# Optimization experiments

Hardware: AMD Instinct MI355X
Metric: run time of the kernel (lower is better)

Reference implementation:

```python
import jax, jax.numpy as jnp
import numpy as np

B, T, D = 1, 2048, 1024
H = 16
SEM_DIM, GEO_DIM, ATTN_DIM = 512, 512, 1024
ROPE_BASE = 10000.0
NEG = -1e9


def setup_inputs() -> dict:
    key = jax.random.key(0)
    ks = jax.random.split(key, 10)
    s = 0.02
    return {
        "x": jax.random.normal(ks[0], (B, T, D), jnp.float32),
        "wq_sem": jax.random.normal(ks[1], (D, SEM_DIM), jnp.float32) * s,
        "wk_sem": jax.random.normal(ks[2], (D, SEM_DIM), jnp.float32) * s,
        "wq_geo": jax.random.normal(ks[3], (D, GEO_DIM), jnp.float32) * s,
        "wk_geo": jax.random.normal(ks[4], (D, GEO_DIM), jnp.float32) * s,
        "wv": jax.random.normal(ks[5], (D, ATTN_DIM), jnp.float32) * s,
        "wo": jax.random.normal(ks[6], (ATTN_DIM, D), jnp.float32) * s,
        "k_sem_null": jax.random.normal(ks[7], (SEM_DIM,), jnp.float32) * s,
        "k_geo_null": jax.random.normal(ks[8], (GEO_DIM,), jnp.float32) * s,
        "v_null": jax.random.normal(ks[9], (ATTN_DIM,), jnp.float32) * s,
    }


def _heads(y, hd):
    b, t, _ = y.shape
    return y.reshape(b, t, H, hd).transpose(0, 2, 1, 3)  # [B,H,T,hd]


def _rope(x, cos, sin):
    # x: [B,H,T,hd], cos/sin: [T,hd//2] (rotate-half convention)
    hd = x.shape[-1]
    x1, x2 = x[..., : hd // 2], x[..., hd // 2 :]
    c = cos[None, None]
    sn = sin[None, None]
    return jnp.concatenate([x1 * c - x2 * sn, x2 * c + x1 * sn], axis=-1)


def _forward(x, wq_sem, wk_sem, wq_geo, wk_geo, wv, wo, k_sem_null, k_geo_null, v_null):
    b, t, _ = x.shape
    sem_hd = wq_sem.shape[1] // H
    geo_hd = wq_geo.shape[1] // H
    v_hd = wv.shape[1] // H
    sem_scale = 1.0 / np.sqrt(sem_hd)
    geo_scale = 1.0 / np.sqrt(geo_hd)

    qs = _heads(x @ wq_sem, sem_hd)
    ks = _heads(x @ wk_sem, sem_hd)
    qg = _heads(x @ wq_geo, geo_hd)
    kg = _heads(x @ wk_geo, geo_hd)
    v = _heads(x @ wv, v_hd)

    # RoPE on geometric branch only
    pos = jnp.arange(t, dtype=jnp.float32)
    inv_freq = 1.0 / (ROPE_BASE ** (jnp.arange(0, geo_hd, 2, dtype=jnp.float32) / geo_hd))
    ang = pos[:, None] * inv_freq[None, :]  # [T, geo_hd//2]
    cos, sin = jnp.cos(ang), jnp.sin(ang)
    qg = _rope(qg, cos, sin)
    kg = _rope(kg, cos, sin)

    # prepend null KV slot (not rotated, always attendable)
    ksn = jnp.broadcast_to(k_sem_null.reshape(1, 1, H, sem_hd).transpose(0, 2, 1, 3), (b, H, 1, sem_hd))
    kgn = jnp.broadcast_to(k_geo_null.reshape(1, 1, H, geo_hd).transpose(0, 2, 1, 3), (b, H, 1, geo_hd))
    vn = jnp.broadcast_to(v_null.reshape(1, 1, H, v_hd).transpose(0, 2, 1, 3), (b, H, 1, v_hd))
    ks_full = jnp.concatenate([ksn, ks], axis=2)  # [B,H,T+1,sem_hd]
    kg_full = jnp.concatenate([kgn, kg], axis=2)
    v_full = jnp.concatenate([vn, v], axis=2)

    # decoupled scores in fp32: sem*sem_scale + geo*geo_scale
    scores = (
        jnp.einsum("bhqd,bhkd->bhqk", qs, ks_full).astype(jnp.float32) * sem_scale
        + jnp.einsum("bhqd,bhkd->bhqk", qg, kg_full).astype(jnp.float32) * geo_scale
    )

    # causal mask over real tokens; null slot (key index 0) always visible
    causal = jnp.tril(jnp.ones((t, t), dtype=bool))
    mask = jnp.concatenate([jnp.ones((t, 1), dtype=bool), causal], axis=1)  # [T, T+1]
    scores = jnp.where(mask[None, None], scores, NEG)

    probs = jax.nn.softmax(scores, axis=-1).astype(v.dtype)
    out = jnp.einsum("bhqk,bhkd->bhqd", probs, v_full)  # [B,H,T,v_hd]
    out = out.transpose(0, 2, 1, 3).reshape(b, t, H * v_hd)
    return out @ wo


def reference(x, wq_sem, wk_sem, wq_geo, wk_geo, wv, wo, k_sem_null, k_geo_null, v_null):
    return _forward(x, wq_sem, wk_sem, wq_geo, wk_geo, wv, wo, k_sem_null, k_geo_null, v_null)
```

## Files before the change

### kernel.cpp

```cpp
#include <hip/hip_runtime.h>
#include <hip/hip_bf16.h>

typedef __hip_bfloat16 bf16;
typedef __attribute__((ext_vector_type(8))) short bf16x8;
typedef __attribute__((ext_vector_type(4))) short bf16x4;
typedef __attribute__((ext_vector_type(4))) float f32x4;

#define TSEQ   2048
#define DMODEL 1024
#define NHEAD  16
#define KST    2112
#define SCALE  0.17677669529663687f
#define LN1E4_16 0.5756462732485115f

__device__ __forceinline__ unsigned short f2bf(float f) {
    union { bf16 h; unsigned short u; } x;
    x.h = __float2bfloat16(f);
    return x.u;
}
__device__ __forceinline__ float bf2f(unsigned short u) {
    return __uint_as_float(((unsigned int)u) << 16);
}

__device__ __forceinline__ void gload_lds16(const void* g, void* l) {
    __builtin_amdgcn_global_load_lds(
        (const __attribute__((address_space(1))) void*)g,
        (__attribute__((address_space(3))) void*)l, 16, 0, 0);
}

__global__ __launch_bounds__(256) void convert_x(const float* __restrict__ X,
                                                 unsigned short* __restrict__ Xb)
{
    int i = (blockIdx.x * 256 + threadIdx.x) * 4;
    float4 v = *(const float4*)(X + i);
    ushort4 o;
    o.x = f2bf(v.x); o.y = f2bf(v.y); o.z = f2bf(v.z); o.w = f2bf(v.w);
    *(ushort4*)(Xb + i) = o;
}

__global__ __launch_bounds__(256) void transpose_all(
    const float* __restrict__ wqs, const float* __restrict__ wks,
    const float* __restrict__ wqg, const float* __restrict__ wkg,
    const float* __restrict__ wv,  const float* __restrict__ wo,
    unsigned short* __restrict__ WcatT, unsigned short* __restrict__ WoT)
{
    __shared__ float T[64][65];
    const float* src; unsigned short* dst; int C;
    switch (blockIdx.z) {
        case 0: src = wqs; dst = WcatT;               C = 512;  break;
        case 1: src = wks; dst = WcatT + 512  * 1024; C = 512;  break;
        case 2: src = wqg; dst = WcatT + 1024 * 1024; C = 512;  break;
        case 3: src = wkg; dst = WcatT + 1536 * 1024; C = 512;  break;
        case 4: src = wv;  dst = WcatT + 2048 * 1024; C = 1024; break;
        default: src = wo; dst = WoT;                 C = 1024; break;
    }
    const int c0 = blockIdx.x * 64;
    if (c0 >= C) return;
    const int r0 = blockIdx.y * 64;
    const int tid = threadIdx.x;
    #pragma unroll
    for (int i = 0; i < 16; ++i) {
        int idx = tid + 256 * i;
        int r = idx >> 6, c = idx & 63;
        T[r][c] = src[(size_t)(r0 + r) * C + c0 + c];
    }
    __syncthreads();
    #pragma unroll
    for (int i = 0; i < 16; ++i) {
        int idx = tid + 256 * i;
        int cc = idx >> 6, rr = idx & 63;
        dst[(size_t)(c0 + cc) * 1024 + r0 + rr] = f2bf(T[rr][cc]);
    }
}

__global__ __launch_bounds__(256) void init_null(
    const float* __restrict__ ksn, const float* __restrict__ kgn,
    const float* __restrict__ vn,
    unsigned short* __restrict__ Kc, unsigned short* __restrict__ Vg)
{
    const int h = blockIdx.x;
    const int tid = threadIdx.x;
    const int d = tid & 63, g = tid >> 6;
    if (g == 0)
        Kc[((size_t)h * KST + 0) * 64 + d] =
            f2bf(d < 32 ? ksn[h * 32 + d] : kgn[h * 32 + d - 32]);
    if (g == 1)
        Vg[((size_t)h * 64 + d) * KST + 0] = f2bf(vn[h * 64 + d]);
    for (int fk = 2049 + g; fk < KST; fk += 4) {
        Kc[((size_t)h * KST + fk) * 64 + d] = 0;
        Vg[((size_t)h * 64 + d) * KST + fk] = 0;
    }
}

__global__ __launch_bounds__(256) void gemm_proj_fused(
    const unsigned short* __restrict__ A,
    const unsigned short* __restrict__ Bt,
    unsigned short* __restrict__ Qc,
    unsigned short* __restrict__ Kc,
    unsigned short* __restrict__ Vg)
{
    __shared__ __align__(16) unsigned short Abuf[64 * 32];
    __shared__ __align__(16) unsigned short Bbuf[128 * 32];
    const int n0 = blockIdx.x * 128, m0 = blockIdx.y * 64;
    const int tid = threadIdx.x, l = tid & 63, wv = tid >> 6;
    const int wr = wv >> 1, wc = wv & 1;
    const int lr = l & 15, lg = l >> 4, kf = lg * 8;

    const int arow = wv * 16 + (l >> 2);
    const int aseg = (l & 3) * 8;

    f32x4 acc[2][4];
    #pragma unroll
    for (int i = 0; i < 2; ++i)
        #pragma unroll
        for (int j = 0; j < 4; ++j) acc[i][j] = (f32x4){0.f, 0.f, 0.f, 0.f};

    for (int k0 = 0; k0 < 1024; k0 += 32) {
        gload_lds16(A + (size_t)(m0 + arow) * 1024 + k0 + aseg, &Abuf[wv * 512]);
        #pragma unroll
        for (int it = 0; it < 2; ++it) {
            int brow = it * 64 + wv * 16 + (l >> 2);
            gload_lds16(Bt + (size_t)(n0 + brow) * 1024 + k0 + aseg,
                        &Bbuf[(it * 256 + wv * 64) * 8]);
        }
        __syncthreads();
        bf16x8 af[2], bfv[4];
        #pragma unroll
        for (int mf = 0; mf < 2; ++mf)
            af[mf] = *(const bf16x8*)&Abuf[(wr * 32 + mf * 16 + lr) * 32 + kf];
        #pragma unroll
        for (int nf = 0; nf < 4; ++nf)
            bfv[nf] = *(const bf16x8*)&Bbuf[(wc * 64 + nf * 16 + lr) * 32 + kf];
        #pragma unroll
        for (int mf = 0; mf < 2; ++mf)
            #pragma unroll
            for (int nf = 0; nf < 4; ++nf)
                acc[mf][nf] = __builtin_amdgcn_mfma_f32_16x16x32_bf16(
                    af[mf], bfv[nf], acc[mf][nf], 0, 0, 0);
        __syncthreads();
    }

    const int sec = n0 >> 9;
    if (sec <= 1) {
        unsigned short* dst = (sec == 0) ? Qc : Kc;
        const int tstr  = (sec == 0) ? TSEQ : KST;
        const int fkoff = (sec == 0) ? 0 : 1;
        const float sc  = (sec == 0) ? SCALE : 1.0f;
        #pragma unroll
        for (int mf = 0; mf < 2; ++mf)
            #pragma unroll
            for (int nf = 0; nf < 4; ++nf) {
                int col = (n0 & 511) + wc * 64 + nf * 16 + lr;
                int h = col >> 5, d = col & 31;
                #pragma unroll
                for (int reg = 0; reg < 4; ++reg) {
                    int q = m0 + wr * 32 + mf * 16 + lg * 4 + reg;
                    dst[((size_t)h * tstr + q + fkoff) * 64 + d] =
                        f2bf(acc[mf][nf][reg] * sc);
                }
            }
    } else if (sec <= 3) {
        unsigned short* dst = (sec == 2) ? Qc : Kc;
        const int tstr  = (sec == 2) ? TSEQ : KST;
        const int fkoff = (sec == 2) ? 0 : 1;
        const float sc  = (sec == 2) ? SCALE : 1.0f;
        const float invf = __expf(-(float)lr * LN1E4_16);
        #pragma unroll
        for (int mf = 0; mf < 2; ++mf)
            #pragma unroll
            for (int reg = 0; reg < 4; ++reg) {
                int q = m0 + wr * 32 + mf * 16 + lg * 4 + reg;
                float s, c;
                __sincosf((float)q * invf, &s, &c);
                #pragma unroll
                for (int nfp = 0; nfp < 2; ++nfp) {
                    int nf0 = nfp * 2;
                    int colbase = (n0 & 511) + wc * 64 + nf0 * 16;
                    int h = colbase >> 5;
                    float x1 = acc[mf][nf0][reg], x2 = acc[mf][nf0 + 1][reg];
                    size_t base = ((size_t)h * tstr + q + fkoff) * 64 + 32;
                    dst[base + lr]      = f2bf((x1 * c - x2 * s) * sc);
                    dst[base + lr + 16] = f2bf((x2 * c + x1 * s) * sc);
                }
            }
    } else {
        #pragma unroll
        for (int nf = 0; nf < 4; ++nf) {
            int colr = (n0 - 2048) + wc * 64 + nf * 16 + lr;
            int h = colr >> 6, dv = colr & 63;
            size_t rowbase = ((size_t)h * 64 + dv) * KST;
            #pragma unroll
            for (int mf = 0; mf < 2; ++mf)
                #pragma unroll
                for (int reg = 0; reg < 4; ++reg) {
                    int q = m0 + wr * 32 + mf * 16 + lg * 4 + reg;
                    Vg[rowbase + q + 1] = f2bf(acc[mf][nf][reg]);
                }
        }
    }
}

__global__ __launch_bounds__(256) void gemm_out(const unsigned short* __restrict__ A,
                                                const unsigned short* __restrict__ Bt,
                                                float* __restrict__ C)
{
    __shared__ __align__(16) unsigned short Abuf[64 * 32];
    __shared__ __align__(16) unsigned short Bbuf[64 * 32];
    const int n0 = blockIdx.x * 64, m0 = blockIdx.y * 64;
    const int tid = threadIdx.x, l = tid & 63, wv = tid >> 6;
    const int wr = wv >> 1, wc = wv & 1;
    const int lr = l & 15, lg = l >> 4, kf = lg * 8;

    const int arow = wv * 16 + (l >> 2);
    const int aseg = (l & 3) * 8;

    f32x4 acc[2][2];
    #pragma unroll
    for (int i = 0; i < 2; ++i)
        #pragma unroll
        for (int j = 0; j < 2; ++j) acc[i][j] = (f32x4){0.f, 0.f, 0.f, 0.f};

    for (int k0 = 0; k0 < 1024; k0 += 32) {
        gload_lds16(A  + (size_t)(m0 + arow) * 1024 + k0 + aseg, &Abuf[wv * 512]);
        gload_lds16(Bt + (size_t)(n0 + arow) * 1024 + k0 + aseg, &Bbuf[wv * 512]);
        __syncthreads();
        bf16x8 af[2], bfv[2];
        #pragma unroll
        for (int mf = 0; mf < 2; ++mf)
            af[mf] = *(const bf16x8*)&Abuf[(wr * 32 + mf * 16 + lr) * 32 + kf];
        #pragma unroll
        for (int nf = 0; nf < 2; ++nf)
            bfv[nf] = *(const bf16x8*)&Bbuf[(wc * 32 + nf * 16 + lr) * 32 + kf];
        #pragma unroll
        for (int mf = 0; mf < 2; ++mf)
            #pragma unroll
            for (int nf = 0; nf < 2; ++nf)
                acc[mf][nf] = __builtin_amdgcn_mfma_f32_16x16x32_bf16(
                    af[mf], bfv[nf], acc[mf][nf], 0, 0, 0);
        __syncthreads();
    }
    #pragma unroll
    for (int mf = 0; mf < 2; ++mf)
        #pragma unroll
        for (int nf = 0; nf < 2; ++nf)
            #pragma unroll
            for (int reg = 0; reg < 4; ++reg) {
                int row = m0 + wr * 32 + mf * 16 + lg * 4 + reg;
                int col = n0 + wc * 32 + nf * 16 + lr;
                C[(size_t)row * DMODEL + col] = acc[mf][nf][reg];
            }
}

__global__ __launch_bounds__(256) void attn_mfma(
    const unsigned short* __restrict__ Qc,
    const unsigned short* __restrict__ Kc,
    const unsigned short* __restrict__ Vg,
    unsigned short* __restrict__ attnO,
    unsigned short* __restrict__ Opart,
    float2* __restrict__ ml)
{
    __shared__ __align__(16) unsigned short KsL[2][64 * 64];
    __shared__ __align__(16) unsigned short VsL[2][64 * 64];
    __shared__ __align__(16) unsigned short Ps[64 * 64];

    const int h = blockIdx.y;
    int qb, t0, t1, part;
    bool split;
    {
        int i = blockIdx.x;
        if (i < 32) {
            split = true; qb = 31 - (i >> 1); part = i & 1;
            int nk = qb + 2, half = nk >> 1;
            t0 = part ? half : 0;
            t1 = part ? nk : half;
        } else {
            split = false; qb = 47 - i; part = 0;
            t0 = 0; t1 = qb + 2;
        }
    }
    const int q0 = qb * 64;
    const int tid = threadIdx.x, l = tid & 63, w = tid >> 6;
    const int lr = l & 15, lg = l >> 4;

    const int qrow = q0 + w * 16 + lr;
    const int d0 = lg * 8;
    bf16x8 qa0 = *(const bf16x8*)&Qc[((size_t)h * TSEQ + qrow) * 64 + d0];
    bf16x8 qa1 = *(const bf16x8*)&Qc[((size_t)h * TSEQ + qrow) * 64 + 32 + d0];

    const int sc8 = (((l & 7) ^ ((l >> 3) & 7))) * 8;
    const int r0s = (w * 2 + 0) * 8 + (l >> 3);
    const int r1s = (w * 2 + 1) * 8 + (l >> 3);
    const unsigned short* Kh = Kc + (((size_t)h * KST) << 6);
    const unsigned short* Vh = Vg + (size_t)h * 64 * KST;

#define STAGE_KV(bufi, fk0_) do {                                              \
        gload_lds16(Kh + (((size_t)((fk0_) + r0s)) << 6) + sc8,                \
                    &KsL[bufi][(w * 2 + 0) * 512]);                            \
        gload_lds16(Kh + (((size_t)((fk0_) + r1s)) << 6) + sc8,                \
                    &KsL[bufi][(w * 2 + 1) * 512]);                            \
        gload_lds16(Vh + (size_t)r0s * KST + (fk0_) + sc8,                     \
                    &VsL[bufi][(w * 2 + 0) * 512]);                            \
        gload_lds16(Vh + (size_t)r1s * KST + (fk0_) + sc8,                     \
                    &VsL[bufi][(w * 2 + 1) * 512]);                            \
    } while (0)

    f32x4 o[4];
    #pragma unroll
    for (int i = 0; i < 4; ++i) o[i] = (f32x4){0.f, 0.f, 0.f, 0.f};
    float m = -1e30f, ll = 0.0f;
    const int q = qrow;

    int buf = 0;
    STAGE_KV(0, t0 * 64);
    asm volatile("s_waitcnt vmcnt(0)" ::: "memory");
    __builtin_amdgcn_s_barrier();

    for (int kb = t0; kb < t1; ++kb) {
        const int fk0 = kb * 64;
        if (kb + 1 < t1) STAGE_KV(buf ^ 1, fk0 + 64);

        const unsigned short* Ksb = &KsL[buf][0];
        const unsigned short* Vsb = &VsL[buf][0];

        f32x4 sa[4];
        #pragma unroll
        for (int i = 0; i < 4; ++i) sa[i] = (f32x4){0.f, 0.f, 0.f, 0.f};
        __builtin_amdgcn_s_setprio(1);
        #pragma unroll
        for (int ks = 0; ks < 2; ++ks) {
            int dd = lg * 8 + ks * 32;
            bf16x8 qa = ks ? qa1 : qa0;
            #pragma unroll
            for (int nf = 0; nf < 4; ++nf) {
                int kkc = nf * 16 + lr;
                bf16x8 kbf = *(const bf16x8*)&Ksb[kkc * 64 + (dd ^ ((kkc & 7) << 3))];
                sa[nf] = __builtin_amdgcn_mfma_f32_16x16x32_bf16(kbf, qa, sa[nf], 0, 0, 0);
            }
        }
        __builtin_amdgcn_s_setprio(0);

        float sv[4][4];
        float mt = -1e30f;
        #pragma unroll
        for (int nf = 0; nf < 4; ++nf)
            #pragma unroll
            for (int reg = 0; reg < 4; ++reg) {
                int fk = fk0 + nf * 16 + lg * 4 + reg;
                float val = (fk <= q + 1) ? sa[nf][reg] : -1e9f;
                sv[nf][reg] = val;
                mt = fmaxf(mt, val);
            }
        mt = fmaxf(mt, __shfl_xor(mt, 16, 64));
        mt = fmaxf(mt, __shfl_xor(mt, 32, 64));
        float mn = fmaxf(m, mt);
        float alpha = __expf(m - mn);
        m = mn;
        float rs = 0.0f;
        #pragma unroll
        for (int nf = 0; nf < 4; ++nf)
            #pragma unroll
            for (int reg = 0; reg < 4; ++reg) {
                float p = __expf(sv[nf][reg] - m);
                sv[nf][reg] = p;
                rs += p;
            }
        rs += __shfl_xor(rs, 16, 64);
        rs += __shfl_xor(rs, 32, 64);
        ll = ll * alpha + rs;
        #pragma unroll
        for (int nf = 0; nf < 4; ++nf)
            #pragma unroll
            for (int reg = 0; reg < 4; ++reg)
                o[nf][reg] *= alpha;

        {
            int r = w * 16 + lr;
            #pragma unroll
            for (int nf = 0; nf < 4; ++nf) {
                bf16x4 pk;
                pk[0] = f2bf(sv[nf][0]); pk[1] = f2bf(sv[nf][1]);
                pk[2] = f2bf(sv[nf][2]); pk[3] = f2bf(sv[nf][3]);
                int kk0 = nf * 16 + lg * 4;
                *(bf16x4*)&Ps[r * 64 + (kk0 ^ ((r & 7) << 3))] = pk;
            }
        }

        __builtin_amdgcn_s_setprio(1);
        #pragma unroll
        for (int ks = 0; ks < 2; ++ks) {
            int kk0 = lg * 8 + ks * 32;
            int pr  = w * 16 + lr;
            bf16x8 pa = *(const bf16x8*)&Ps[pr * 64 + (kk0 ^ ((pr & 7) << 3))];
            #pragma unroll
            for (int nf = 0; nf < 4; ++nf) {
                int dv = nf * 16 + lr;
                bf16x8 vb = *(const bf16x8*)&Vsb[dv * 64 + (kk0 ^ ((dv & 7) << 3))];
                o[nf] = __builtin_amdgcn_mfma_f32_16x16x32_bf16(vb, pa, o[nf], 0, 0, 0);
            }
        }
        __builtin_amdgcn_s_setprio(0);

        asm volatile("s_waitcnt vmcnt(0)" ::: "memory");
        __builtin_amdgcn_s_barrier();
        buf ^= 1;
    }
#undef STAGE_KV

    const float inv = 1.0f / ll;
    if (!split) {
        #pragma unroll
        for (int nf = 0; nf < 4; ++nf)
            #pragma unroll
            for (int reg = 0; reg < 4; ++reg) {
                int dv = nf * 16 + lg * 4 + reg;
                attnO[(size_t)q * DMODEL + h * 64 + dv] = f2bf(o[nf][reg] * inv);
            }
    } else {
        const int sidx = (h * 16 + (qb - 16)) * 2 + part;
        unsigned short* Od = Opart + (size_t)sidx * 4096;
        const int r = w * 16 + lr;
        #pragma unroll
        for (int nf = 0; nf < 4; ++nf)
            #pragma unroll
            for (int reg = 0; reg < 4; ++reg) {
                int dv = nf * 16 + lg * 4 + reg;
                Od[r * 64 + dv] = f2bf(o[nf][reg] * inv);
            }
        if (lg == 0)
            ml[sidx * 64 + r] = make_float2(m, ll);
    }
}

__global__ __launch_bounds__(256) void combine_split(
    const unsigned short* __restrict__ Opart,
    const float2* __restrict__ ml,
    unsigned short* __restrict__ attnO)
{
    const int h = blockIdx.x >> 4, qs = blockIdx.x & 15;
    const int qb = 16 + qs;
    const int base = (h * 16 + qs) * 2;
    const unsigned short* O0 = Opart + (size_t)base * 4096;
    const unsigned short* O1 = O0 + 4096;
    const float2* ml0 = ml + base * 64;
    const float2* ml1 = ml0 + 64;
    const int t = threadIdx.x;
    const int dv = t & 63, rg = t >> 6;
    #pragma unroll
    for (int i = 0; i < 16; ++i) {
        int r = rg + i * 4;
        float2 a = ml0[r], b = ml1[r];
        float mm = fmaxf(a.x, b.x);
        float w0 = a.y * __expf(a.x - mm);
        float w1 = b.y * __expf(b.x - mm);
        float inv = 1.0f / (w0 + w1);
        float o0 = bf2f(O0[r * 64 + dv]);
        float o1 = bf2f(O1[r * 64 + dv]);
        int qq = qb * 64 + r;
        attnO[(size_t)qq * DMODEL + h * 64 + dv] = f2bf((w0 * o0 + w1 * o1) * inv);
    }
}

extern "C" void kernel_launch(void* const* d_in, const int* in_sizes, int n_in,
                              void* d_out, int out_size, void* d_ws, size_t ws_size,
                              hipStream_t stream)
{
    const float* x      = (const float*)d_in[0];
    const float* wq_sem = (const float*)d_in[1];
    const float* wk_sem = (const float*)d_in[2];
    const float* wq_geo = (const float*)d_in[3];
    const float* wk_geo = (const float*)d_in[4];
    const float* wv     = (const float*)d_in[5];
    const float* wo     = (const float*)d_in[6];
    const float* ksn    = (const float*)d_in[7];
    const float* kgn    = (const float*)d_in[8];
    const float* vn     = (const float*)d_in[9];
    float* out = (float*)d_out;

    char* ws = (char*)d_ws;
    unsigned short* Xb    = (unsigned short*)(ws);
    unsigned short* attnO = (unsigned short*)(ws);
    unsigned short* WcatT = (unsigned short*)(ws + 4194304);
    unsigned short* WoT   = (unsigned short*)(ws + 10485760);
    unsigned short* Qc    = (unsigned short*)(ws + 12582912);
    unsigned short* Kc    = (unsigned short*)(ws + 16777216);
    unsigned short* Vg    = (unsigned short*)(ws + 21102592);
    unsigned short* Opart = (unsigned short*)(ws + 25427968);
    float2*         ml    = (float2*)(ws + 29622272);

    convert_x<<<2048, 256, 0, stream>>>(x, Xb);
    transpose_all<<<dim3(16, 16, 6), 256, 0, stream>>>(
        wq_sem, wk_sem, wq_geo, wk_geo, wv, wo, WcatT, WoT);
    init_null<<<16, 256, 0, stream>>>(ksn, kgn, vn, Kc, Vg);

    gemm_proj_fused<<<dim3(24, 32), 256, 0, stream>>>(Xb, WcatT, Qc, Kc, Vg);

    attn_mfma<<<dim3(48, NHEAD), 256, 0, stream>>>(Qc, Kc, Vg, attnO, Opart, ml);
    combine_split<<<256, 256, 0, stream>>>(Opart, ml, attnO);

    gemm_out<<<dim3(16, 32), 256, 0, stream>>>(attnO, WoT, out);
}
```

Baseline: 97.32 us.

## Restructure attention into independent per-wave 16-row tasks with 1-3 way KV splits

```diff
diff --git a/kernel.cpp b/kernel.cpp
--- a/kernel.cpp
+++ b/kernel.cpp
@@ -251,7 +251,7 @@
             }
 }
 
-__global__ __launch_bounds__(256) void attn_mfma(
+__global__ __launch_bounds__(256, 3) void attn_wave(
     const unsigned short* __restrict__ Qc,
     const unsigned short* __restrict__ Kc,
     const unsigned short* __restrict__ Vg,
@@ -259,68 +259,59 @@
     unsigned short* __restrict__ Opart,
     float2* __restrict__ ml)
 {
-    __shared__ __align__(16) unsigned short KsL[2][64 * 64];
-    __shared__ __align__(16) unsigned short VsL[2][64 * 64];
-    __shared__ __align__(16) unsigned short Ps[64 * 64];
-
-    const int h = blockIdx.y;
-    int qb, t0, t1, part;
-    bool split;
-    {
-        int i = blockIdx.x;
-        if (i < 32) {
-            split = true; qb = 31 - (i >> 1); part = i & 1;
-            int nk = qb + 2, half = nk >> 1;
-            t0 = part ? half : 0;
-            t1 = part ? nk : half;
-        } else {
-            split = false; qb = 47 - i; part = 0;
-            t0 = 0; t1 = qb + 2;
-        }
-    }
-    const int q0 = qb * 64;
+    __shared__ __align__(16) unsigned short Ps[4][16 * 64];
+
     const int tid = threadIdx.x, l = tid & 63, w = tid >> 6;
     const int lr = l & 15, lg = l >> 4;
 
-    const int qrow = q0 + w * 16 + lr;
-    const int d0 = lg * 8;
-    bf16x8 qa0 = *(const bf16x8*)&Qc[((size_t)h * TSEQ + qrow) * 64 + d0];
-    bf16x8 qa1 = *(const bf16x8*)&Qc[((size_t)h * TSEQ + qrow) * 64 + 32 + d0];
-
-    const int sc8 = (((l & 7) ^ ((l >> 3) & 7))) * 8;
-    const int r0s = (w * 2 + 0) * 8 + (l >> 3);
-    const int r1s = (w * 2 + 1) * 8 + (l >> 3);
+    const int g = blockIdx.x * 4 + w;
+    const int h = g & 15;
+    const int p = 253 - (g >> 4);
+    int qsl, part, nparts;
+    if (p < 43)       { qsl = p; part = 0; nparts = 1; }
+    else if (p < 131) { int j = p - 43; qsl = 43 + (j >> 1); part = j & 1; nparts = 2; }
+    else              { int j = p - 131; qsl = 87 + j / 3; part = j % 3; nparts = 3; }
+
+    const int nt = (qsl + 1) / 4 + 1;
+    const int base = nt / nparts, rem = nt % nparts;
+    const int t0 = part * base + (part < rem ? part : rem);
+    const int t1 = t0 + base + (part < rem ? 1 : 0);
+
+    const int q = qsl * 16 + lr;
+
+    bf16x8 qa0 = *(const bf16x8*)&Qc[((size_t)h * TSEQ + q) * 64 + lg * 8];
+    bf16x8 qa1 = *(const bf16x8*)&Qc[((size_t)h * TSEQ + q) * 64 + 32 + lg * 8];
+
     const unsigned short* Kh = Kc + (((size_t)h * KST) << 6);
     const unsigned short* Vh = Vg + (size_t)h * 64 * KST;
 
-#define STAGE_KV(bufi, fk0_) do {                                              \
-        gload_lds16(Kh + (((size_t)((fk0_) + r0s)) << 6) + sc8,                \
-                    &KsL[bufi][(w * 2 + 0) * 512]);                            \
-        gload_lds16(Kh + (((size_t)((fk0_) + r1s)) << 6) + sc8,                \
-                    &KsL[bufi][(w * 2 + 1) * 512]);                            \
-        gload_lds16(Vh + (size_t)r0s * KST + (fk0_) + sc8,                     \
-                    &VsL[bufi][(w * 2 + 0) * 512]);                            \
-        gload_lds16(Vh + (size_t)r1s * KST + (fk0_) + sc8,                     \
-                    &VsL[bufi][(w * 2 + 1) * 512]);                            \
+    bf16x8 kr[8], vr[8];
+#define LOADK(fk0_) do {                                                       \
+        _Pragma("unroll")                                                      \
+        for (int ks = 0; ks < 2; ++ks)                                         \
+            _Pragma("unroll")                                                  \
+            for (int nf = 0; nf < 4; ++nf)                                     \
+                kr[ks * 4 + nf] = *(const bf16x8*)                             \
+                    &Kh[(size_t)((fk0_) + nf * 16 + lr) * 64 + lg * 8 + ks * 32]; \
+    } while (0)
+#define LOADV(fk0_) do {                                                       \
+        _Pragma("unroll")                                                      \
+        for (int ks = 0; ks < 2; ++ks)                                         \
+            _Pragma("unroll")                                                  \
+            for (int nf = 0; nf < 4; ++nf)                                     \
+                vr[ks * 4 + nf] = *(const bf16x8*)                             \
+                    &Vh[(size_t)(nf * 16 + lr) * KST + (fk0_) + lg * 8 + ks * 32]; \
     } while (0)
 
     f32x4 o[4];
     #pragma unroll
     for (int i = 0; i < 4; ++i) o[i] = (f32x4){0.f, 0.f, 0.f, 0.f};
     float m = -1e30f, ll = 0.0f;
-    const int q = qrow;
-
-    int buf = 0;
-    STAGE_KV(0, t0 * 64);
-    asm volatile("s_waitcnt vmcnt(0)" ::: "memory");
-    __builtin_amdgcn_s_barrier();
-
+
+    LOADK(t0 * 64);
     for (int kb = t0; kb < t1; ++kb) {
         const int fk0 = kb * 64;
-        if (kb + 1 < t1) STAGE_KV(buf ^ 1, fk0 + 64);
-
-        const unsigned short* Ksb = &KsL[buf][0];
-        const unsigned short* Vsb = &VsL[buf][0];
+        LOADV(fk0);
 
         f32x4 sa[4];
         #pragma unroll
@@ -328,14 +319,11 @@
         __builtin_amdgcn_s_setprio(1);
         #pragma unroll
         for (int ks = 0; ks < 2; ++ks) {
-            int dd = lg * 8 + ks * 32;
             bf16x8 qa = ks ? qa1 : qa0;
             #pragma unroll
-            for (int nf = 0; nf < 4; ++nf) {
-                int kkc = nf * 16 + lr;
-                bf16x8 kbf = *(const bf16x8*)&Ksb[kkc * 64 + (dd ^ ((kkc & 7) << 3))];
-                sa[nf] = __builtin_amdgcn_mfma_f32_16x16x32_bf16(kbf, qa, sa[nf], 0, 0, 0);
-            }
+            for (int nf = 0; nf < 4; ++nf)
+                sa[nf] = __builtin_amdgcn_mfma_f32_16x16x32_bf16(
+                    kr[ks * 4 + nf], qa, sa[nf], 0, 0, 0);
         }
         __builtin_amdgcn_s_setprio(0);
 
@@ -360,9 +348,9 @@
         for (int nf = 0; nf < 4; ++nf)
             #pragma unroll
             for (int reg = 0; reg < 4; ++reg) {
-                float p = __expf(sv[nf][reg] - m);
-                sv[nf][reg] = p;
-                rs += p;
+                float pv = __expf(sv[nf][reg] - m);
+                sv[nf][reg] = pv;
+                rs += pv;
             }
         rs += __shfl_xor(rs, 16, 64);
         rs += __shfl_xor(rs, 32, 64);
@@ -373,91 +361,98 @@
             for (int reg = 0; reg < 4; ++reg)
                 o[nf][reg] *= alpha;
 
+        #pragma unroll
+        for (int nf = 0; nf < 4; ++nf) {
+            bf16x4 pk;
+            pk[0] = f2bf(sv[nf][0]); pk[1] = f2bf(sv[nf][1]);
+            pk[2] = f2bf(sv[nf][2]); pk[3] = f2bf(sv[nf][3]);
+            int kk0 = nf * 16 + lg * 4;
+            *(bf16x4*)&Ps[w][lr * 64 + (kk0 ^ ((lr & 7) << 3))] = pk;
+        }
+
         {
-            int r = w * 16 + lr;
-            #pragma unroll
-            for (int nf = 0; nf < 4; ++nf) {
-                bf16x4 pk;
-                pk[0] = f2bf(sv[nf][0]); pk[1] = f2bf(sv[nf][1]);
-                pk[2] = f2bf(sv[nf][2]); pk[3] = f2bf(sv[nf][3]);
-                int kk0 = nf * 16 + lg * 4;
-                *(bf16x4*)&Ps[r * 64 + (kk0 ^ ((r & 7) << 3))] = pk;
-            }
+            int tn = (kb + 1 < t1) ? kb + 1 : kb;
+            LOADK(tn * 64);
         }
 
         __builtin_amdgcn_s_setprio(1);
         #pragma unroll
         for (int ks = 0; ks < 2; ++ks) {
             int kk0 = lg * 8 + ks * 32;
-            int pr  = w * 16 + lr;
-            bf16x8 pa = *(const bf16x8*)&Ps[pr * 64 + (kk0 ^ ((pr & 7) << 3))];
-            #pragma unroll
-            for (int nf = 0; nf < 4; ++nf) {
-                int dv = nf * 16 + lr;
-                bf16x8 vb = *(const bf16x8*)&Vsb[dv * 64 + (kk0 ^ ((dv & 7) << 3))];
-                o[nf] = __builtin_amdgcn_mfma_f32_16x16x32_bf16(vb, pa, o[nf], 0, 0, 0);
-            }
+            bf16x8 pa = *(const bf16x8*)&Ps[w][lr * 64 + (kk0 ^ ((lr & 7) << 3))];
+            #pragma unroll
+            for (int nf = 0; nf < 4; ++nf)
+                o[nf] = __builtin_amdgcn_mfma_f32_16x16x32_bf16(
+                    vr[ks * 4 + nf], pa, o[nf], 0, 0, 0);
         }
         __builtin_amdgcn_s_setprio(0);
-
-        asm volatile("s_waitcnt vmcnt(0)" ::: "memory");
-        __builtin_amdgcn_s_barrier();
-        buf ^= 1;
-    }
-#undef STAGE_KV
-
-    const float inv = 1.0f / ll;
-    if (!split) {
-        #pragma unroll
-        for (int nf = 0; nf < 4; ++nf)
-            #pragma unroll
-            for (int reg = 0; reg < 4; ++reg) {
-                int dv = nf * 16 + lg * 4 + reg;
-                attnO[(size_t)q * DMODEL + h * 64 + dv] = f2bf(o[nf][reg] * inv);
-            }
+    }
+#undef LOADK
+#undef LOADV
+
+    const float invl = 1.0f / ll;
+    if (nparts == 1) {
+        #pragma unroll
+        for (int nf = 0; nf < 4; ++nf) {
+            ushort4 ov;
+            ov.x = f2bf(o[nf][0] * invl); ov.y = f2bf(o[nf][1] * invl);
+            ov.z = f2bf(o[nf][2] * invl); ov.w = f2bf(o[nf][3] * invl);
+            *(ushort4*)&attnO[(size_t)q * DMODEL + h * 64 + nf * 16 + lg * 4] = ov;
+        }
     } else {
-        const int sidx = (h * 16 + (qb - 16)) * 2 + part;
-        unsigned short* Od = Opart + (size_t)sidx * 4096;
-        const int r = w * 16 + lr;
-        #pragma unroll
-        for (int nf = 0; nf < 4; ++nf)
-            #pragma unroll
-            for (int reg = 0; reg < 4; ++reg) {
-                int dv = nf * 16 + lg * 4 + reg;
-                Od[r * 64 + dv] = f2bf(o[nf][reg] * inv);
-            }
+        int local = (nparts == 2) ? (qsl - 43) * 2 + part
+                                  : 88 + (qsl - 87) * 3 + part;
+        int sidx = h * 211 + local;
+        unsigned short* Od = Opart + (size_t)sidx * 1024;
+        #pragma unroll
+        for (int nf = 0; nf < 4; ++nf) {
+            ushort4 ov;
+            ov.x = f2bf(o[nf][0] * invl); ov.y = f2bf(o[nf][1] * invl);
+            ov.z = f2bf(o[nf][2] * invl); ov.w = f2bf(o[nf][3] * invl);
+            *(ushort4*)&Od[lr * 64 + nf * 16 + lg * 4] = ov;
+        }
         if (lg == 0)
-            ml[sidx * 64 + r] = make_float2(m, ll);
-    }
-}
-
-__global__ __launch_bounds__(256) void combine_split(
+            ml[sidx * 16 + lr] = make_float2(m, ll);
+    }
+}
+
+__global__ __launch_bounds__(256) void combine_wave(
     const unsigned short* __restrict__ Opart,
     const float2* __restrict__ ml,
     unsigned short* __restrict__ attnO)
 {
-    const int h = blockIdx.x >> 4, qs = blockIdx.x & 15;
-    const int qb = 16 + qs;
-    const int base = (h * 16 + qs) * 2;
-    const unsigned short* O0 = Opart + (size_t)base * 4096;
-    const unsigned short* O1 = O0 + 4096;
-    const float2* ml0 = ml + base * 64;
-    const float2* ml1 = ml0 + 64;
+    const int bx = blockIdx.x;
+    const int h = bx / 85, qsl = 43 + bx % 85;
+    const int nparts = (qsl < 87) ? 2 : 3;
+    const int local0 = (qsl < 87) ? (qsl - 43) * 2 : 88 + (qsl - 87) * 3;
+    const int sidx0 = h * 211 + local0;
     const int t = threadIdx.x;
-    const int dv = t & 63, rg = t >> 6;
-    #pragma unroll
-    for (int i = 0; i < 16; ++i) {
-        int r = rg + i * 4;
-        float2 a = ml0[r], b = ml1[r];
-        float mm = fmaxf(a.x, b.x);
-        float w0 = a.y * __expf(a.x - mm);
-        float w1 = b.y * __expf(b.x - mm);
-        float inv = 1.0f / (w0 + w1);
-        float o0 = bf2f(O0[r * 64 + dv]);
-        float o1 = bf2f(O1[r * 64 + dv]);
-        int qq = qb * 64 + r;
-        attnO[(size_t)qq * DMODEL + h * 64 + dv] = f2bf((w0 * o0 + w1 * o1) * inv);
-    }
+    const int r = t >> 4, dv0 = (t & 15) * 4;
+
+    float2 m0 = ml[(sidx0 + 0) * 16 + r];
+    float2 m1 = ml[(sidx0 + 1) * 16 + r];
+    float2 m2 = (nparts == 3) ? ml[(sidx0 + 2) * 16 + r] : make_float2(-1e30f, 0.f);
+    float mm = fmaxf(fmaxf(m0.x, m1.x), m2.x);
+    float w0 = m0.y * __expf(m0.x - mm);
+    float w1 = m1.y * __expf(m1.x - mm);
+    float w2 = m2.y * __expf(m2.x - mm);
+    float inv = 1.0f / (w0 + w1 + w2);
+
+    const unsigned short* O0 = Opart + (size_t)(sidx0 + 0) * 1024 + r * 64 + dv0;
+    const unsigned short* O1 = Opart + (size_t)(sidx0 + 1) * 1024 + r * 64 + dv0;
+    const unsigned short* O2 = (nparts == 3)
+        ? Opart + (size_t)(sidx0 + 2) * 1024 + r * 64 + dv0 : O0;
+
+    ushort4 a = *(const ushort4*)O0;
+    ushort4 b = *(const ushort4*)O1;
+    ushort4 c = *(const ushort4*)O2;
+    ushort4 ov;
+    ov.x = f2bf((w0 * bf2f(a.x) + w1 * bf2f(b.x) + w2 * bf2f(c.x)) * inv);
+    ov.y = f2bf((w0 * bf2f(a.y) + w1 * bf2f(b.y) + w2 * bf2f(c.y)) * inv);
+    ov.z = f2bf((w0 * bf2f(a.z) + w1 * bf2f(b.z) + w2 * bf2f(c.z)) * inv);
+    ov.w = f2bf((w0 * bf2f(a.w) + w1 * bf2f(b.w) + w2 * bf2f(c.w)) * inv);
+    int q = qsl * 16 + r;
+    *(ushort4*)&attnO[(size_t)q * DMODEL + h * 64 + dv0] = ov;
 }
 
 extern "C" void kernel_launch(void* const* d_in, const int* in_sizes, int n_in,
@@ -485,7 +480,7 @@
     unsigned short* Kc    = (unsigned short*)(ws + 16777216);
     unsigned short* Vg    = (unsigned short*)(ws + 21102592);
     unsigned short* Opart = (unsigned short*)(ws + 25427968);
-    float2*         ml    = (float2*)(ws + 29622272);
+    float2*         ml    = (float2*)(ws + 32342016);
 
     convert_x<<<2048, 256, 0, stream>>>(x, Xb);
     transpose_all<<<dim3(16, 16, 6), 256, 0, stream>>>(
@@ -494,8 +489,8 @@
 
     gemm_proj_fused<<<dim3(24, 32), 256, 0, stream>>>(Xb, WcatT, Qc, Kc, Vg);
 
-    attn_mfma<<<dim3(48, NHEAD), 256, 0, stream>>>(Qc, Kc, Vg, attnO, Opart, ml);
-    combine_split<<<256, 256, 0, stream>>>(Opart, ml, attnO);
+    attn_wave<<<1016, 256, 0, stream>>>(Qc, Kc, Vg, attnO, Opart, ml);
+    combine_wave<<<16 * 85, 256, 0, stream>>>(Opart, ml, attnO);
 
     gemm_out<<<dim3(16, 32), 256, 0, stream>>>(attnO, WoT, out);
 }
```

Result: slower. 140.4 us (+44.3%).

## Split long causal query blocks into up to four KV partitions and skip lazy rescales

Applied to the files above, without the earlier changes.

```diff
diff --git a/kernel.cpp b/kernel.cpp
--- a/kernel.cpp
+++ b/kernel.cpp
@@ -256,7 +256,8 @@
     const unsigned short* __restrict__ Kc,
     const unsigned short* __restrict__ Vg,
     unsigned short* __restrict__ attnO,
-    unsigned short* __restrict__ Opart,
+    unsigned short* __restrict__ OpA,
+    unsigned short* __restrict__ OpB,
     float2* __restrict__ ml)
 {
     __shared__ __align__(16) unsigned short KsL[2][64 * 64];
@@ -264,28 +265,26 @@
     __shared__ __align__(16) unsigned short Ps[64 * 64];
 
     const int h = blockIdx.y;
-    int qb, t0, t1, part;
-    bool split;
+    int qb, part, np;
     {
         int i = blockIdx.x;
-        if (i < 32) {
-            split = true; qb = 31 - (i >> 1); part = i & 1;
-            int nk = qb + 2, half = nk >> 1;
-            t0 = part ? half : 0;
-            t1 = part ? nk : half;
-        } else {
-            split = false; qb = 47 - i; part = 0;
-            t0 = 0; t1 = qb + 2;
-        }
-    }
+        if (i < 24)      { np = 4; qb = 31 - (i >> 2); part = i & 3; }
+        else if (i < 51) { int j = i - 24; np = 3; qb = 25 - j / 3; part = j % 3; }
+        else if (i < 69) { int j = i - 51; np = 2; qb = 16 - (j >> 1); part = j & 1; }
+        else             { np = 1; qb = 7 - (blockIdx.x - 69); part = 0; }
+    }
+    const int nt = qb + 2;
+    const int base = nt / np, rem = nt % np;
+    const int t0 = part * base + (part < rem ? part : rem);
+    const int t1 = t0 + base + (part < rem ? 1 : 0);
+
     const int q0 = qb * 64;
     const int tid = threadIdx.x, l = tid & 63, w = tid >> 6;
     const int lr = l & 15, lg = l >> 4;
 
     const int qrow = q0 + w * 16 + lr;
-    const int d0 = lg * 8;
-    bf16x8 qa0 = *(const bf16x8*)&Qc[((size_t)h * TSEQ + qrow) * 64 + d0];
-    bf16x8 qa1 = *(const bf16x8*)&Qc[((size_t)h * TSEQ + qrow) * 64 + 32 + d0];
+    bf16x8 qa0 = *(const bf16x8*)&Qc[((size_t)h * TSEQ + qrow) * 64 + lg * 8];
+    bf16x8 qa1 = *(const bf16x8*)&Qc[((size_t)h * TSEQ + qrow) * 64 + 32 + lg * 8];
 
     const int sc8 = (((l & 7) ^ ((l >> 3) & 7))) * 8;
     const int r0s = (w * 2 + 0) * 8 + (l >> 3);
@@ -352,9 +351,17 @@
             }
         mt = fmaxf(mt, __shfl_xor(mt, 16, 64));
         mt = fmaxf(mt, __shfl_xor(mt, 32, 64));
-        float mn = fmaxf(m, mt);
-        float alpha = __expf(m - mn);
-        m = mn;
+        if (__any(mt > m + 8.0f)) {
+            float mn = fmaxf(m, mt);
+            float alpha = __expf(m - mn);
+            m = mn;
+            ll *= alpha;
+            #pragma unroll
+            for (int nf = 0; nf < 4; ++nf)
+                #pragma unroll
+                for (int reg = 0; reg < 4; ++reg)
+                    o[nf][reg] *= alpha;
+        }
         float rs = 0.0f;
         #pragma unroll
         for (int nf = 0; nf < 4; ++nf)
@@ -366,12 +373,7 @@
             }
         rs += __shfl_xor(rs, 16, 64);
         rs += __shfl_xor(rs, 32, 64);
-        ll = ll * alpha + rs;
-        #pragma unroll
-        for (int nf = 0; nf < 4; ++nf)
-            #pragma unroll
-            for (int reg = 0; reg < 4; ++reg)
-                o[nf][reg] *= alpha;
+        ll += rs;
 
         {
             int r = w * 16 + lr;
@@ -407,7 +409,7 @@
 #undef STAGE_KV
 
     const float inv = 1.0f / ll;
-    if (!split) {
+    if (np == 1) {
         #pragma unroll
         for (int nf = 0; nf < 4; ++nf)
             #pragma unroll
@@ -416,8 +418,10 @@
                 attnO[(size_t)q * DMODEL + h * 64 + dv] = f2bf(o[nf][reg] * inv);
             }
     } else {
-        const int sidx = (h * 16 + (qb - 16)) * 2 + part;
-        unsigned short* Od = Opart + (size_t)sidx * 4096;
+        const int sidx = h * 69 + blockIdx.x;
+        unsigned short* Od = (sidx < 768)
+            ? OpA + (size_t)sidx * 4096
+            : OpB + (size_t)(sidx - 768) * 4096;
         const int r = w * 16 + lr;
         #pragma unroll
         for (int nf = 0; nf < 4; ++nf)
@@ -431,32 +435,74 @@
     }
 }
 
-__global__ __launch_bounds__(256) void combine_split(
-    const unsigned short* __restrict__ Opart,
+__global__ __launch_bounds__(256) void combine_wave(
+    const unsigned short* __restrict__ OpA,
+    const unsigned short* __restrict__ OpB,
     const float2* __restrict__ ml,
     unsigned short* __restrict__ attnO)
 {
-    const int h = blockIdx.x >> 4, qs = blockIdx.x & 15;
-    const int qb = 16 + qs;
-    const int base = (h * 16 + qs) * 2;
-    const unsigned short* O0 = Opart + (size_t)base * 4096;
-    const unsigned short* O1 = O0 + 4096;
-    const float2* ml0 = ml + base * 64;
-    const float2* ml1 = ml0 + 64;
+    const int qb = 8 + blockIdx.x;
+    const int h  = blockIdx.y;
+    int np, i0;
+    if (qb >= 26)      { np = 4; i0 = (31 - qb) * 4; }
+    else if (qb >= 17) { np = 3; i0 = 24 + (25 - qb) * 3; }
+    else               { np = 2; i0 = 51 + (16 - qb) * 2; }
+    const int sidx0 = h * 69 + i0;
+
     const int t = threadIdx.x;
-    const int dv = t & 63, rg = t >> 6;
-    #pragma unroll
-    for (int i = 0; i < 16; ++i) {
-        int r = rg + i * 4;
-        float2 a = ml0[r], b = ml1[r];
-        float mm = fmaxf(a.x, b.x);
-        float w0 = a.y * __expf(a.x - mm);
-        float w1 = b.y * __expf(b.x - mm);
-        float inv = 1.0f / (w0 + w1);
-        float o0 = bf2f(O0[r * 64 + dv]);
-        float o1 = bf2f(O1[r * 64 + dv]);
-        int qq = qb * 64 + r;
-        attnO[(size_t)qq * DMODEL + h * 64 + dv] = f2bf((w0 * o0 + w1 * o1) * inv);
+    const int r = t >> 2, dv0 = (t & 3) * 16;
+
+    float wt[4];
+    float mm = -1e30f;
+    #pragma unroll
+    for (int p = 0; p < 4; ++p) {
+        wt[p] = 0.0f;
+        if (p < np) {
+            float2 v = ml[(sidx0 + p) * 64 + r];
+            wt[p] = v.x;
+            mm = fmaxf(mm, v.x);
+        }
+    }
+    float tot = 0.0f;
+    #pragma unroll
+    for (int p = 0; p < 4; ++p) {
+        if (p < np) {
+            float2 v = ml[(sidx0 + p) * 64 + r];
+            wt[p] = v.y * __expf(v.x - mm);
+            tot += wt[p];
+        }
+    }
+    const float inv = 1.0f / tot;
+
+    float accv[16];
+    #pragma unroll
+    for (int c = 0; c < 16; ++c) accv[c] = 0.0f;
+    #pragma unroll
+    for (int p = 0; p < 4; ++p) {
+        if (p < np) {
+            int s = sidx0 + p;
+            const unsigned short* Od = (s < 768)
+                ? OpA + (size_t)s * 4096
+                : OpB + (size_t)(s - 768) * 4096;
+            #pragma unroll
+            for (int c4 = 0; c4 < 4; ++c4) {
+                ushort4 v = *(const ushort4*)&Od[r * 64 + dv0 + c4 * 4];
+                accv[c4 * 4 + 0] += wt[p] * bf2f(v.x);
+                accv[c4 * 4 + 1] += wt[p] * bf2f(v.y);
+                accv[c4 * 4 + 2] += wt[p] * bf2f(v.z);
+                accv[c4 * 4 + 3] += wt[p] * bf2f(v.w);
+            }
+        }
+    }
+    const int q = qb * 64 + r;
+    #pragma unroll
+    for (int c4 = 0; c4 < 4; ++c4) {
+        ushort4 ov;
+        ov.x = f2bf(accv[c4 * 4 + 0] * inv);
+        ov.y = f2bf(accv[c4 * 4 + 1] * inv);
+        ov.z = f2bf(accv[c4 * 4 + 2] * inv);
+        ov.w = f2bf(accv[c4 * 4 + 3] * inv);
+        *(ushort4*)&attnO[(size_t)q * DMODEL + h * 64 + dv0 + c4 * 4] = ov;
     }
 }
 
@@ -480,12 +526,13 @@
     unsigned short* Xb    = (unsigned short*)(ws);
     unsigned short* attnO = (unsigned short*)(ws);
     unsigned short* WcatT = (unsigned short*)(ws + 4194304);
+    unsigned short* OpA   = (unsigned short*)(ws + 4194304);
     unsigned short* WoT   = (unsigned short*)(ws + 10485760);
     unsigned short* Qc    = (unsigned short*)(ws + 12582912);
     unsigned short* Kc    = (unsigned short*)(ws + 16777216);
     unsigned short* Vg    = (unsigned short*)(ws + 21102592);
-    unsigned short* Opart = (unsigned short*)(ws + 25427968);
-    float2*         ml    = (float2*)(ws + 29622272);
+    unsigned short* OpB   = (unsigned short*)(ws + 25427968);
+    float2*         ml    = (float2*)(ws + 28180480);
 
     convert_x<<<2048, 256, 0, stream>>>(x, Xb);
     transpose_all<<<dim3(16, 16, 6), 256, 0, stream>>>(
@@ -494,8 +541,8 @@
 
     gemm_proj_fused<<<dim3(24, 32), 256, 0, stream>>>(Xb, WcatT, Qc, Kc, Vg);
 
-    attn_mfma<<<dim3(48, NHEAD), 256, 0, stream>>>(Qc, Kc, Vg, attnO, Opart, ml);
-    combine_split<<<256, 256, 0, stream>>>(Opart, ml, attnO);
+    attn_mfma<<<dim3(77, NHEAD), 256, 0, stream>>>(Qc, Kc, Vg, attnO, OpA, OpB, ml);
+    combine_wave<<<dim3(24, NHEAD), 256, 0, stream>>>(OpA, OpB, ml, attnO);
 
     gemm_out<<<dim3(16, 32), 256, 0, stream>>>(attnO, WoT, out);
 }
```

Result: faster. 95.32 us (-2.1%).
